# Optimization experiments

Hardware: AMD Instinct MI355X
Metric: run time of the kernel (lower is better)

Reference implementation:

```python
import jax, jax.numpy as jnp
import numpy as np

PATCH = 64      # patch_size
K = 16          # num_patches
UNF_K = 16      # unfold kernel
UNF_S = 8       # unfold stride


def setup_inputs() -> dict:
    key = jax.random.key(0)
    k0, k1, k2 = jax.random.split(key, 3)
    B, C, H, W = 32, 3, 384, 384
    x = jax.random.normal(k0, (B, C, H, W), dtype=jnp.float32)
    # encoder params: Conv2d(3,32,3,s2,p1) -> ReLU -> Conv2d(32,64,3,s2,p1) -> GAP
    w1 = jax.random.normal(k1, (32, 3, 3, 3), dtype=jnp.float32) * 0.1
    b1 = jnp.zeros((32,), dtype=jnp.float32)
    w2 = jax.random.normal(k2, (64, 32, 3, 3), dtype=jnp.float32) * 0.05
    b2 = jnp.zeros((64,), dtype=jnp.float32)
    return {"x": x, "w1": w1, "b1": b1, "w2": w2, "b2": b2}


def _patch_variances(x):
    # torch.var(unfold(x,16,8), dim=1), unbiased, over C*16*16 = 768 elems.
    # Computed via window sums instead of materializing the unfold tensor.
    win = (1, 1, UNF_K, UNF_K)
    st = (1, 1, UNF_S, UNF_S)
    s = jax.lax.reduce_window(x, 0.0, jax.lax.add, win, st, 'VALID')
    s2 = jax.lax.reduce_window(x * x, 0.0, jax.lax.add, win, st, 'VALID')
    s = s.sum(axis=1)    # [B, gh, gw]
    s2 = s2.sum(axis=1)  # [B, gh, gw]
    n = x.shape[1] * UNF_K * UNF_K  # 768
    var = (s2 - s * s / n) / (n - 1)
    return var.reshape(var.shape[0], -1)  # [B, gh*gw], row-major like F.unfold


def _encode(patches, w1, b1, w2, b2):
    # patches: [N, 3, 64, 64] -> [N, 64]
    dn = ('NCHW', 'OIHW', 'NCHW')
    y = jax.lax.conv_general_dilated(patches, w1, (2, 2), [(1, 1), (1, 1)],
                                     dimension_numbers=dn) + b1[None, :, None, None]
    y = jax.nn.relu(y)
    y = jax.lax.conv_general_dilated(y, w2, (2, 2), [(1, 1), (1, 1)],
                                     dimension_numbers=dn) + b2[None, :, None, None]
    return y.mean(axis=(2, 3))  # AdaptiveAvgPool2d(1)


def reference(x, w1, b1, w2, b2):
    B, C, H, W = x.shape
    var = _patch_variances(x)                 # [B, L]
    _, idx = jax.lax.top_k(var, K)            # [B, K]
    # faithful (buggy) decode from the source: divisor is W//8, step 8
    h = (idx // (W // UNF_S)) * UNF_S         # [B, K]
    w = (idx % (W // UNF_S)) * UNF_S          # [B, K]

    def slice_one(img, hh, ww):
        # dynamic_slice clamps starts so the 64x64 crop stays in-bounds
        return jax.lax.dynamic_slice(img, (0, hh, ww), (C, PATCH, PATCH))

    gather = jax.vmap(lambda img, hs, ws: jax.vmap(
        lambda hh, ww: slice_one(img, hh, ww))(hs, ws))
    patches = gather(x, h, w)                 # [B, K, 3, 64, 64]
    feats = _encode(patches.reshape(B * K, C, PATCH, PATCH), w1, b1, w2, b2)
    return feats.reshape(B, K, -1).mean(axis=1)  # [B, 64]
```

## Files before the change

kernel.cpp:

```cpp
#include <hip/hip_runtime.h>
#include <math.h>

#define NB 32
#define GH 47
#define GW 47
#define NWIN (GH*GW)
#define KSEL 16
#define RPITCH 17
#define SEG 48

__global__ __launch_bounds__(256) void k_var(const float* __restrict__ x,
                                             float* __restrict__ var)
{
    __shared__ double hs [3][24][SEG];
    __shared__ double hs2[3][24][SEG];
    int gyp = blockIdx.x;
    int b   = blockIdx.y;
    int tid = threadIdx.x;
    int R0  = gyp * 16;

    for (int tau = tid; tau < 3*24*SEG; tau += 256) {
        int sg = tau % SEG;
        int t2 = tau / SEG;
        int rr = t2 % 24;
        int c  = t2 / 24;
        int row = R0 + rr;
        double s = 0.0, s2 = 0.0;
        if (row < 384) {
            const float* px = x + (((size_t)(b*3 + c)*384 + row)*384 + sg*8);
            #pragma unroll
            for (int q = 0; q < 2; ++q) {
                float4 v = *reinterpret_cast<const float4*>(px + q*4);
                double a0 = v.x, a1 = v.y, a2 = v.z, a3 = v.w;
                s  += a0 + a1 + a2 + a3;
                s2 = fma(a0,a0, fma(a1,a1, fma(a2,a2, fma(a3,a3, s2))));
            }
        }
        hs [c][rr][sg] = s;
        hs2[c][rr][sg] = s2;
    }
    __syncthreads();

    if (tid < 188) {
        int which = tid & 1;
        int rest  = tid >> 1;
        int gx = rest % 47, g = rest / 47;
        int gy = gyp*2 + g;
        if (gy < GH) {
            const double* base = which ? &hs2[0][0][0] : &hs[0][0][0];
            double S = 0.0;
            #pragma unroll
            for (int c = 0; c < 3; ++c)
                #pragma unroll
                for (int r = 0; r < 16; ++r) {
                    const double* rp = base + ((c*24) + (g*8 + r))*SEG + gx;
                    S += rp[0] + rp[1];
                }
            double P = __shfl_xor(S, 1, 64);
            if (which == 0) {
                var[(size_t)b*NWIN + gy*GW + gx] =
                    (float)((P - S*S/768.0) / 767.0);
            }
        }
    }
}

__global__ __launch_bounds__(256) void k_topk(const float* __restrict__ var,
                                              int* __restrict__ coords)
{
    __shared__ float lv[NWIN];
    __shared__ float s_val[4];
    __shared__ int   s_idx[4];
    __shared__ int   chosen[KSEL];
    int b = blockIdx.x, tid = threadIdx.x;
    int lane = tid & 63, wavid = tid >> 6;

    for (int i = tid; i < NWIN; i += 256) lv[i] = var[(size_t)b*NWIN + i];
    __syncthreads();

    for (int k = 0; k < KSEL; ++k) {
        float bv = -INFINITY; int bi = NWIN;
        for (int i = tid; i < NWIN; i += 256) {
            float v = lv[i];
            if (v > bv) { bv = v; bi = i; }
        }
        #pragma unroll
        for (int m = 1; m < 64; m <<= 1) {
            float ov = __shfl_xor(bv, m, 64);
            int   oi = __shfl_xor(bi, m, 64);
            if (ov > bv || (ov == bv && oi < bi)) { bv = ov; bi = oi; }
        }
        if (lane == 0) { s_val[wavid] = bv; s_idx[wavid] = bi; }
        __syncthreads();
        if (tid == 0) {
            float cv = s_val[0]; int ci = s_idx[0];
            #pragma unroll
            for (int wv = 1; wv < 4; ++wv) {
                if (s_val[wv] > cv || (s_val[wv] == cv && s_idx[wv] < ci)) {
                    cv = s_val[wv]; ci = s_idx[wv];
                }
            }
            chosen[k] = ci;
            lv[ci] = -INFINITY;
        }
        __syncthreads();
    }

    if (tid < KSEL) {
        int idx = chosen[tid];
        int h = (idx / 48) * 8; if (h > 320) h = 320;
        int w = (idx % 48) * 8; if (w > 320) w = 320;
        coords[(b*KSEL + tid)*2 + 0] = h;
        coords[(b*KSEL + tid)*2 + 1] = w;
    }
}

__global__ __launch_bounds__(1024, 1) void k_encode(const float* __restrict__ x,
    const float* __restrict__ w1, const float* __restrict__ b1,
    const int* __restrict__ coords, float* __restrict__ sbuf)
{
    __shared__ float4 sin4[3*66*RPITCH];
    __shared__ float  s_part[16][2][4][3];
    __shared__ float  s_c31[8][4][3];

    int p    = blockIdx.x;
    int bimg = p >> 4;
    int tid  = threadIdx.x;
    int h0 = coords[p*2 + 0];
    int w0 = coords[p*2 + 1];

    float* sinf = (float*)sin4;

    if (tid < 243) {
        int c = tid / 81, j = tid - c*81;
        if (j < 17) {
            sin4[(c*66 + 0)*RPITCH + j] = make_float4(0.f, 0.f, 0.f, 0.f);
        } else {
            int r  = j - 16;
            int sw = (r >> 1) & 7;
            sinf[((c*66 + r)*RPITCH + sw)*4] = 0.f;
        }
    }

    #pragma unroll
    for (int it = 0; it < 3; ++it) {
        int fi  = tid + it*1024;
        int c   = fi >> 10;
        int rem = fi & 1023;
        int y   = rem >> 4;
        int x4  = rem & 15;
        float4 v = *reinterpret_cast<const float4*>(
            x + (((size_t)(bimg*3 + c)*384 + (h0 + y))*384 + w0 + x4*4));
        int r  = y + 1;
        int sw = (r >> 1) & 7;
        float vals[4] = {v.x, v.y, v.z, v.w};
        #pragma unroll
        for (int e = 0; e < 4; ++e) {
            int pcol = x4*4 + 1 + e;
            int k  = pcol >> 2, bb = pcol & 3;
            int ks = (k < 16) ? ((k & 8) | ((k & 7) ^ sw)) : 16;
            sinf[((c*66 + r)*RPITCH + ks)*4 + bb] = vals[e];
        }
    }
    __syncthreads();

    int wave = tid >> 6;
    int lane = tid & 63;
    int sub  = wave & 1;
    int icq  = __builtin_amdgcn_readfirstlane(tid >> 7);
    int iy   = sub*16 + (lane >> 2);
    int xq   = lane & 3;

    float acc[4][8];
    #pragma unroll
    for (int i = 0; i < 4; ++i)
        #pragma unroll
        for (int u = 0; u < 8; ++u) acc[i][u] = 0.f;

    const float* w1g = w1 + icq*4*27;

    for (int ch = 0; ch < 3; ++ch) {
        for (int ky = 0; ky < 3; ++ky) {
            int r    = 2*iy + ky;
            int sw   = (r >> 1) & 7;
            int base = (ch*66 + r)*RPITCH;
            float s[17];
            #pragma unroll
            for (int j = 0; j < 4; ++j) {
                int k = 4*xq + j;
                float4 v = sin4[base + ((k & 8) | ((k & 7) ^ sw))];
                s[4*j+0] = v.x; s[4*j+1] = v.y; s[4*j+2] = v.z; s[4*j+3] = v.w;
            }
            {
                int k  = 4*xq + 4;
                int ks = (k < 16) ? ((k & 8) | ((k & 7) ^ sw)) : 16;
                s[16] = sinf[(base + ks)*4];
            }
            const float* wp = w1g + ch*9 + ky*3;
            #pragma unroll
            for (int i = 0; i < 4; ++i) {
                float wA = wp[i*27 + 0];
                float wB = wp[i*27 + 1];
                float wC = wp[i*27 + 2];
                #pragma unroll
                for (int u = 0; u < 8; ++u)
                    acc[i][u] = fmaf(s[2*u], wA,
                                 fmaf(s[2*u+1], wB,
                                  fmaf(s[2*u+2], wC, acc[i][u])));
            }
        }
    }

    float R[4][3];
    #pragma unroll
    for (int i = 0; i < 4; ++i) {
        float bias = b1[icq*4 + i];
        float c1 = 0.f, c2 = 0.f, v7 = 0.f;
        #pragma unroll
        for (int u = 0; u < 8; ++u) {
            float v = fmaxf(acc[i][u] + bias, 0.f);
            if (u & 1) c2 += v; else c1 += v;
            if (u == 7) v7 = v;
        }
        R[i][0] = c2 - ((xq == 3) ? v7 : 0.f);
        R[i][1] = c1;
        R[i][2] = c2;
    }

    #pragma unroll
    for (int m = 1; m <= 2; m <<= 1)
        #pragma unroll
        for (int i = 0; i < 4; ++i)
            #pragma unroll
            for (int k = 0; k < 3; ++k)
                R[i][k] += __shfl_xor(R[i][k], m, 64);

    float c31[4][3];
    #pragma unroll
    for (int i = 0; i < 4; ++i)
        #pragma unroll
        for (int k = 0; k < 3; ++k)
            c31[i][k] = __shfl(R[i][k], 60, 64);

    #pragma unroll
    for (int m = 8; m < 64; m <<= 1)
        #pragma unroll
        for (int i = 0; i < 4; ++i)
            #pragma unroll
            for (int k = 0; k < 3; ++k)
                R[i][k] += __shfl_xor(R[i][k], m, 64);

    if (lane == 0) {
        #pragma unroll
        for (int i = 0; i < 4; ++i)
            #pragma unroll
            for (int k = 0; k < 3; ++k)
                s_part[wave][0][i][k] = R[i][k];
    } else if (lane == 4) {
        #pragma unroll
        for (int i = 0; i < 4; ++i)
            #pragma unroll
            for (int k = 0; k < 3; ++k)
                s_part[wave][1][i][k] = R[i][k];
    }
    if (sub == 1 && lane == 8) {
        #pragma unroll
        for (int i = 0; i < 4; ++i)
            #pragma unroll
            for (int k = 0; k < 3; ++k)
                s_c31[icq][i][k] = c31[i][k];
    }
    __syncthreads();

    if (tid < 288) {
        int ic = tid / 9, j = tid - ic*9;
        int ky = j / 3, kx = j - ky*3;
        int g = ic >> 2, i = ic & 3;
        float even = s_part[2*g][0][i][kx] + s_part[2*g+1][0][i][kx];
        float odd  = s_part[2*g][1][i][kx] + s_part[2*g+1][1][i][kx];
        float val = (ky == 1) ? even : odd;
        if (ky == 0) val = odd - s_c31[g][i][kx];
        sbuf[(size_t)p*288 + tid] = val;
    }
}

__global__ __launch_bounds__(256) void k_reduce(const float* __restrict__ sbuf,
    const float* __restrict__ w2, const float* __restrict__ b2,
    float* __restrict__ out)
{
    __shared__ float Ssum[288];
    __shared__ float s_part[256];
    int b = blockIdx.x, tid = threadIdx.x;

    for (int i = tid; i < 288; i += 256) {
        float s = 0.f;
        #pragma unroll
        for (int k = 0; k < KSEL; ++k)
            s += sbuf[(size_t)(b*KSEL + k)*288 + i];
        Ssum[i] = s;
    }
    __syncthreads();

    int oc = tid & 63, q = tid >> 6;
    const float4* w4 = reinterpret_cast<const float4*>(w2 + oc*288 + q*72);
    const float4* S4 = reinterpret_cast<const float4*>(Ssum + q*72);
    float a = 0.f;
    #pragma unroll
    for (int t = 0; t < 18; ++t) {
        float4 wv = w4[t];
        float4 sv = S4[t];
        a = fmaf(wv.x, sv.x, fmaf(wv.y, sv.y,
             fmaf(wv.z, sv.z, fmaf(wv.w, sv.w, a))));
    }
    s_part[tid] = a;
    __syncthreads();
    if (tid < 64) {
        float t = s_part[tid] + s_part[64 + tid] + s_part[128 + tid] + s_part[192 + tid];
        out[b*64 + tid] = b2[tid] + t * (1.0f/4096.0f);
    }
}

extern "C" void kernel_launch(void* const* d_in, const int* in_sizes, int n_in,
                              void* d_out, int out_size, void* d_ws, size_t ws_size,
                              hipStream_t stream)
{
    const float* x  = (const float*)d_in[0];
    const float* w1 = (const float*)d_in[1];
    const float* b1 = (const float*)d_in[2];
    const float* w2 = (const float*)d_in[3];
    const float* b2 = (const float*)d_in[4];
    float* out = (float*)d_out;

    char* ws = (char*)d_ws;
    int*   coords = (int*)ws;
    float* var    = (float*)(ws + 4096);
    float* sbuf   = (float*)(ws + 287744);

    k_var   <<<dim3(24, NB), 256, 0, stream>>>(x, var);
    k_topk  <<<NB,           256, 0, stream>>>(var, coords);
    k_encode<<<NB*KSEL,     1024, 0, stream>>>(x, w1, b1, coords, sbuf);
    k_reduce<<<NB,           256, 0, stream>>>(sbuf, w2, b2, out);
}
```

Before: 77.30 us.

## Restructure conv1 encode to register-tiled all-channels per thread without LDS staging

```diff
diff --git a/kernel.cpp b/kernel.cpp
--- a/kernel.cpp
+++ b/kernel.cpp
@@ -6,7 +6,6 @@
 #define GW 47
 #define NWIN (GH*GW)
 #define KSEL 16
-#define RPITCH 17
 #define SEG 48
 
 __global__ __launch_bounds__(256) void k_var(const float* __restrict__ x,
@@ -115,171 +114,107 @@
     }
 }
 
-__global__ __launch_bounds__(1024, 1) void k_encode(const float* __restrict__ x,
+__global__ __launch_bounds__(512) void k_encode(const float* __restrict__ x,
     const float* __restrict__ w1, const float* __restrict__ b1,
     const int* __restrict__ coords, float* __restrict__ sbuf)
 {
-    __shared__ float4 sin4[3*66*RPITCH];
-    __shared__ float  s_part[16][2][4][3];
-    __shared__ float  s_c31[8][4][3];
+    __shared__ float s_part[8][32][3];
+    __shared__ float s_r31[32][3];
 
     int p    = blockIdx.x;
     int bimg = p >> 4;
     int tid  = threadIdx.x;
+    int wave = tid >> 6;
+    int lane = tid & 63;
+    int half = lane >> 5;
+    int ox   = lane & 31;
     int h0 = coords[p*2 + 0];
     int w0 = coords[p*2 + 1];
 
-    float* sinf = (float*)sin4;
-
-    if (tid < 243) {
-        int c = tid / 81, j = tid - c*81;
-        if (j < 17) {
-            sin4[(c*66 + 0)*RPITCH + j] = make_float4(0.f, 0.f, 0.f, 0.f);
-        } else {
-            int r  = j - 16;
-            int sw = (r >> 1) & 7;
-            sinf[((c*66 + r)*RPITCH + sw)*4] = 0.f;
-        }
-    }
-
+    const float* xb = x + (size_t)bimg*3*384*384;
+
+    float S[32];
     #pragma unroll
-    for (int it = 0; it < 3; ++it) {
-        int fi  = tid + it*1024;
-        int c   = fi >> 10;
-        int rem = fi & 1023;
-        int y   = rem >> 4;
-        int x4  = rem & 15;
-        float4 v = *reinterpret_cast<const float4*>(
-            x + (((size_t)(bimg*3 + c)*384 + (h0 + y))*384 + w0 + x4*4));
-        int r  = y + 1;
-        int sw = (r >> 1) & 7;
-        float vals[4] = {v.x, v.y, v.z, v.w};
-        #pragma unroll
-        for (int e = 0; e < 4; ++e) {
-            int pcol = x4*4 + 1 + e;
-            int k  = pcol >> 2, bb = pcol & 3;
-            int ks = (k < 16) ? ((k & 8) | ((k & 7) ^ sw)) : 16;
-            sinf[((c*66 + r)*RPITCH + ks)*4 + bb] = vals[e];
-        }
-    }
-    __syncthreads();
-
-    int wave = tid >> 6;
-    int lane = tid & 63;
-    int sub  = wave & 1;
-    int icq  = __builtin_amdgcn_readfirstlane(tid >> 7);
-    int iy   = sub*16 + (lane >> 2);
-    int xq   = lane & 3;
-
-    float acc[4][8];
+    for (int i = 0; i < 32; ++i) S[i] = 0.f;
+
+    for (int iter = 0; iter < 2; ++iter) {
+        int oy = wave + 8*half + 16*iter;
+
+        float acc[32];
+        #pragma unroll
+        for (int i = 0; i < 32; ++i) acc[i] = 0.f;
+
+        #pragma unroll
+        for (int ch = 0; ch < 3; ++ch) {
+            #pragma unroll
+            for (int ky = 0; ky < 3; ++ky) {
+                int r = 2*oy - 1 + ky;
+                float vx, vy;
+                if (r >= 0) {
+                    float2 v2 = *reinterpret_cast<const float2*>(
+                        xb + ((size_t)ch*384 + (h0 + r))*384 + w0 + 2*ox);
+                    vx = v2.x; vy = v2.y;
+                } else { vx = 0.f; vy = 0.f; }
+                float up = __shfl_up(vy, 1, 64);
+                float vm = (ox == 0) ? 0.f : up;
+                const float* wp = w1 + ch*9 + ky*3;
+                #pragma unroll
+                for (int i = 0; i < 32; ++i) {
+                    float wA = wp[i*27 + 0];
+                    float wB = wp[i*27 + 1];
+                    float wC = wp[i*27 + 2];
+                    acc[i] = fmaf(vm, wA, fmaf(vx, wB, fmaf(vy, wC, acc[i])));
+                }
+            }
+        }
+
+        #pragma unroll
+        for (int i = 0; i < 32; ++i) {
+            float v = fmaxf(acc[i] + b1[i], 0.f);
+            acc[i] = v;
+            S[i] += v;
+        }
+
+        if (iter == 1 && wave == 7) {
+            #pragma unroll
+            for (int i = 0; i < 32; ++i) {
+                float v = half ? acc[i] : 0.f;
+                float c63 = __shfl(v, 63, 64);
+                #pragma unroll
+                for (int m = 2; m <= 32; m <<= 1)
+                    v += __shfl_xor(v, m, 64);
+                if (lane == 0) s_r31[i][1] = v;
+                if (lane == 1) { s_r31[i][2] = v;
+                                 s_r31[i][0] = v - c63; }
+            }
+        }
+    }
+
     #pragma unroll
-    for (int i = 0; i < 4; ++i)
-        #pragma unroll
-        for (int u = 0; u < 8; ++u) acc[i][u] = 0.f;
-
-    const float* w1g = w1 + icq*4*27;
-
-    for (int ch = 0; ch < 3; ++ch) {
-        for (int ky = 0; ky < 3; ++ky) {
-            int r    = 2*iy + ky;
-            int sw   = (r >> 1) & 7;
-            int base = (ch*66 + r)*RPITCH;
-            float s[17];
-            #pragma unroll
-            for (int j = 0; j < 4; ++j) {
-                int k = 4*xq + j;
-                float4 v = sin4[base + ((k & 8) | ((k & 7) ^ sw))];
-                s[4*j+0] = v.x; s[4*j+1] = v.y; s[4*j+2] = v.z; s[4*j+3] = v.w;
-            }
-            {
-                int k  = 4*xq + 4;
-                int ks = (k < 16) ? ((k & 8) | ((k & 7) ^ sw)) : 16;
-                s[16] = sinf[(base + ks)*4];
-            }
-            const float* wp = w1g + ch*9 + ky*3;
-            #pragma unroll
-            for (int i = 0; i < 4; ++i) {
-                float wA = wp[i*27 + 0];
-                float wB = wp[i*27 + 1];
-                float wC = wp[i*27 + 2];
-                #pragma unroll
-                for (int u = 0; u < 8; ++u)
-                    acc[i][u] = fmaf(s[2*u], wA,
-                                 fmaf(s[2*u+1], wB,
-                                  fmaf(s[2*u+2], wC, acc[i][u])));
-            }
-        }
-    }
-
-    float R[4][3];
-    #pragma unroll
-    for (int i = 0; i < 4; ++i) {
-        float bias = b1[icq*4 + i];
-        float c1 = 0.f, c2 = 0.f, v7 = 0.f;
-        #pragma unroll
-        for (int u = 0; u < 8; ++u) {
-            float v = fmaxf(acc[i][u] + bias, 0.f);
-            if (u & 1) c2 += v; else c1 += v;
-            if (u == 7) v7 = v;
-        }
-        R[i][0] = c2 - ((xq == 3) ? v7 : 0.f);
-        R[i][1] = c1;
-        R[i][2] = c2;
-    }
-
-    #pragma unroll
-    for (int m = 1; m <= 2; m <<= 1)
-        #pragma unroll
-        for (int i = 0; i < 4; ++i)
-            #pragma unroll
-            for (int k = 0; k < 3; ++k)
-                R[i][k] += __shfl_xor(R[i][k], m, 64);
-
-    float c31[4][3];
-    #pragma unroll
-    for (int i = 0; i < 4; ++i)
-        #pragma unroll
-        for (int k = 0; k < 3; ++k)
-            c31[i][k] = __shfl(R[i][k], 60, 64);
-
-    #pragma unroll
-    for (int m = 8; m < 64; m <<= 1)
-        #pragma unroll
-        for (int i = 0; i < 4; ++i)
-            #pragma unroll
-            for (int k = 0; k < 3; ++k)
-                R[i][k] += __shfl_xor(R[i][k], m, 64);
-
-    if (lane == 0) {
-        #pragma unroll
-        for (int i = 0; i < 4; ++i)
-            #pragma unroll
-            for (int k = 0; k < 3; ++k)
-                s_part[wave][0][i][k] = R[i][k];
-    } else if (lane == 4) {
-        #pragma unroll
-        for (int i = 0; i < 4; ++i)
-            #pragma unroll
-            for (int k = 0; k < 3; ++k)
-                s_part[wave][1][i][k] = R[i][k];
-    }
-    if (sub == 1 && lane == 8) {
-        #pragma unroll
-        for (int i = 0; i < 4; ++i)
-            #pragma unroll
-            for (int k = 0; k < 3; ++k)
-                s_c31[icq][i][k] = c31[i][k];
+    for (int i = 0; i < 32; ++i) {
+        float v = S[i];
+        float c31 = __shfl(v, 31, 64) + __shfl(v, 63, 64);
+        #pragma unroll
+        for (int m = 2; m <= 32; m <<= 1)
+            v += __shfl_xor(v, m, 64);
+        if (lane == 0) s_part[wave][i][1] = v;
+        if (lane == 1) { s_part[wave][i][2] = v;
+                         s_part[wave][i][0] = v - c31; }
     }
     __syncthreads();
 
     if (tid < 288) {
         int ic = tid / 9, j = tid - ic*9;
         int ky = j / 3, kx = j - ky*3;
-        int g = ic >> 2, i = ic & 3;
-        float even = s_part[2*g][0][i][kx] + s_part[2*g+1][0][i][kx];
-        float odd  = s_part[2*g][1][i][kx] + s_part[2*g+1][1][i][kx];
-        float val = (ky == 1) ? even : odd;
-        if (ky == 0) val = odd - s_c31[g][i][kx];
+        float val;
+        if (ky == 1) {
+            val = s_part[0][ic][kx] + s_part[2][ic][kx]
+                + s_part[4][ic][kx] + s_part[6][ic][kx];
+        } else {
+            float odd = s_part[1][ic][kx] + s_part[3][ic][kx]
+                      + s_part[5][ic][kx] + s_part[7][ic][kx];
+            val = (ky == 2) ? odd : odd - s_r31[ic][kx];
+        }
         sbuf[(size_t)p*288 + tid] = val;
     }
 }
@@ -338,6 +273,6 @@
 
     k_var   <<<dim3(24, NB), 256, 0, stream>>>(x, var);
     k_topk  <<<NB,           256, 0, stream>>>(var, coords);
-    k_encode<<<NB*KSEL,     1024, 0, stream>>>(x, w1, b1, coords, sbuf);
+    k_encode<<<NB*KSEL,      512, 0, stream>>>(x, w1, b1, coords, sbuf);
     k_reduce<<<NB,           256, 0, stream>>>(sbuf, w2, b2, out);
 }
```

Measured after the change: 173.4 us. 2.24x slower.
